# Optimization experiments

Hardware: AMD Instinct MI355X
Metric: run time of the kernel (lower is better)

Reference implementation:

```python
import jax, jax.numpy as jnp
import numpy as np

IN_DIM = 128
HID = 128
OUT = 128

def _linear(x, W, b):
    return x @ W + b

def setup_inputs() -> dict:
    key = jax.random.key(0)
    ks = jax.random.split(key, 16)
    B, N = 2, 512
    def w(k, fan_in, fan_out):
        lim = 1.0 / np.sqrt(fan_in)
        return jax.random.uniform(k, (fan_in, fan_out), jnp.float32, -lim, lim)
    def bvec(k, fan_in, fan_out):
        lim = 1.0 / np.sqrt(fan_in)
        return jax.random.uniform(k, (fan_out,), jnp.float32, -lim, lim)
    return {
        "features": jax.random.normal(ks[0], (B, N, IN_DIM), jnp.float32),
        "coords": jax.random.normal(ks[1], (B, N, 3), jnp.float32),
        "eW1": w(ks[2], 2 * IN_DIM + 1, HID), "eb1": bvec(ks[3], 2 * IN_DIM + 1, HID),
        "eW2": w(ks[4], HID, HID), "eb2": bvec(ks[5], HID, HID),
        "nW1": w(ks[6], IN_DIM + HID, HID), "nb1": bvec(ks[7], IN_DIM + HID, HID),
        "nW2": w(ks[8], HID, OUT), "nb2": bvec(ks[9], HID, OUT),
        "cW1": w(ks[10], HID, HID), "cb1": bvec(ks[11], HID, HID),
        "cW2": w(ks[12], HID, 1), "cb2": bvec(ks[13], HID, 1),
    }

def reference(features, coords, eW1, eb1, eW2, eb2, nW1, nb1, nW2, nb2, cW1, cb1, cW2, cb2):
    B, N, D = features.shape
    # pairwise coordinate differences and distances: (B, N, N, 3), (B, N, N, 1)
    coord_diff = coords[:, :, None, :] - coords[:, None, :, :]
    distances = jnp.sqrt(jnp.sum(coord_diff ** 2, axis=-1, keepdims=True) + 1e-8)
    # all-pairs edge features: (B, N, N, 2D+1)
    feat_i = jnp.broadcast_to(features[:, :, None, :], (B, N, N, D))
    feat_j = jnp.broadcast_to(features[:, None, :, :], (B, N, N, D))
    edge_features = jnp.concatenate([feat_i, feat_j, distances], axis=-1)
    edge_hidden = _linear(jax.nn.silu(_linear(edge_features, eW1, eb1)), eW2, eb2)
    # mean over neighbors j -> (B, N, HID)
    aggregated = jnp.mean(edge_hidden, axis=2)
    node_input = jnp.concatenate([features, aggregated], axis=-1)
    updated_features = _linear(jax.nn.silu(_linear(node_input, nW1, nb1)), nW2, nb2)
    # coordinate update
    coord_weights = _linear(jax.nn.silu(_linear(edge_hidden, cW1, cb1)), cW2, cb2)  # (B,N,N,1)
    updated_coords = coords + jnp.mean(coord_weights * coord_diff, axis=2)
    return (updated_features, updated_coords)
```

## Files before the change

kernel.cpp:

```cpp
#include <hip/hip_runtime.h>
#include <hip/hip_bf16.h>
#include <math.h>


typedef float f32x4 __attribute__((ext_vector_type(4)));
typedef short short8 __attribute__((ext_vector_type(8)));

#define MFMA16(a, b, c) __builtin_amdgcn_mfma_f32_16x16x32_bf16((a), (b), (c), 0, 0, 0)

__device__ __forceinline__ short f2bf(float x) {
    __hip_bfloat16 h = __float2bfloat16(x);
    union { __hip_bfloat16 h; short s; } v; v.h = h;
    return v.s;
}
__device__ __forceinline__ float bf2f(short s) {
    union { unsigned u; float f; } v; v.u = ((unsigned)(unsigned short)s) << 16;
    return v.f;
}
__device__ __forceinline__ float silu_f(float x) {
    return x * __builtin_amdgcn_rcpf(1.0f + __expf(-x));
}

__device__ __forceinline__ int swz(int row, int col) {
    int byte = (row << 8) | (col << 1);
    byte ^= (row & 7) << 4;
    return byte >> 1;
}

__global__ void egnn_prew(const float* __restrict__ feat, const float* __restrict__ eW1,
                          const float* __restrict__ eb1,
                          const float* __restrict__ eW2, const float* __restrict__ cW1,
                          const float* __restrict__ eb2, const float* __restrict__ cb1,
                          float* __restrict__ Abuf, float* __restrict__ Bbuf,
                          unsigned short* __restrict__ MbfT, float* __restrict__ bias2ws,
                          float* __restrict__ aggpart, float* __restrict__ coordpart,
                          int* __restrict__ done) {
    const int bid = blockIdx.x;
    const int t = threadIdx.x;
    if (bid < 1024) {
        __shared__ float f[128];
        if (t < 128) f[t] = feat[bid * 128 + t];
        __syncthreads();
        const int col  = t & 127;
        const int half = t >> 7;
        const float* W = eW1 + (size_t)half * 128 * 128 + col;
        float acc = half ? 0.f : eb1[col];
        #pragma unroll 8
        for (int k = 0; k < 128; ++k) acc += f[k] * W[(size_t)k * 128];
        if (half == 0) Abuf[bid * 128 + col] = acc;
        else           Bbuf[bid * 128 + col] = acc;
        if (t < 128) aggpart[(size_t)bid * 128 + t] = 0.f;
        if (t < 3)   coordpart[bid * 3 + t] = 0.f;
        if (t == 0)  done[bid] = 0;
    } else {
        const int idx = (bid - 1024) * 2 + (t >> 7);
        const int c = t & 127;
        if (idx < 128) {
            float acc = 0.f;
            #pragma unroll 8
            for (int h = 0; h < 128; ++h) acc += eW2[idx * 128 + h] * cW1[h * 128 + c];
            MbfT[c * 128 + idx] = (unsigned short)f2bf(acc);
        } else if (idx == 128) {
            float acc = cb1[c];
            #pragma unroll 8
            for (int h = 0; h < 128; ++h) acc += eb2[h] * cW1[h * 128 + c];
            bias2ws[c] = acc;
        }
    }
}

__global__ void __launch_bounds__(256, 2) egnn_main(
    const float* __restrict__ features, const float* __restrict__ coords,
    const float* __restrict__ eW1, const float* __restrict__ eW2,
    const float* __restrict__ eb2,
    const float* __restrict__ nW1, const float* __restrict__ nb1,
    const float* __restrict__ nW2, const float* __restrict__ nb2,
    const float* __restrict__ cW2, const float* __restrict__ cb2,
    const float* __restrict__ Abuf, const float* __restrict__ Bbuf,
    const unsigned short* __restrict__ MbfT, const float* __restrict__ bias2ws,
    float* __restrict__ aggpart, float* __restrict__ coordpart,
    int* __restrict__ done,
    float* __restrict__ out_feat, float* __restrict__ out_coord)
{
    constexpr int Nn = 512;
    __shared__ __align__(16) short se[64 * 128];
    __shared__ float aw[128], wd[128];
    __shared__ float cdp[2][3][64];
    __shared__ float warr[2][4][64];
    __shared__ float aggred[16][128];
    __shared__ float cred[4][3];
    __shared__ float ci3[3];
    __shared__ float pfi[128], paggh[128], phbuf[128], ppart[128], pcd[3];
    __shared__ int lastflag;

    const int tid  = threadIdx.x;
    const int lane = tid & 63;
    const int wave = tid >> 6;
    const int bid  = blockIdx.x;
    const int node = bid >> 1;
    const int half = bid & 1;
    const int b    = node >> 9;

    if (tid < 128) {
        aw[tid] = Abuf[node * 128 + tid];
        wd[tid] = eW1[256 * 128 + tid];
    }
    if (tid == 0) {
        ci3[0] = coords[node * 3 + 0];
        ci3[1] = coords[node * 3 + 1];
        ci3[2] = coords[node * 3 + 2];
    }

    const int cfrag = wave * 32 + (lane & 15);
    const int koff  = (lane >> 4) * 8;
    short8 wfM[2][4];
    #pragma unroll
    for (int n2 = 0; n2 < 2; ++n2)
        #pragma unroll
        for (int k = 0; k < 4; ++k)
            wfM[n2][k] = *(const short8*)&MbfT[(size_t)(cfrag + n2 * 16) * 128 + k * 32 + koff];
    __syncthreads();

    const float b2_0  = bias2ws[cfrag], b2_1 = bias2ws[cfrag + 16];
    const float cw2_0 = cW2[cfrag],     cw2_1 = cW2[cfrag + 16];
    const float cb2v  = cb2[0];
    const float cix = ci3[0], ciy = ci3[1], ciz = ci3[2];

    const int jr = tid >> 2, cb = (tid & 3) * 32;
    const int rg = tid >> 4, c8 = (tid & 15) * 8;

    float ap[8];
    #pragma unroll
    for (int q = 0; q < 8; ++q) ap[q] = 0.f;
    float cax = 0.f, cay = 0.f, caz = 0.f;

    for (int t = 0; t < 4; ++t) {
        const int par = t & 1;
        {
            const int j = half * 256 + t * 64 + jr;
            const float dx = cix - coords[(b * Nn + j) * 3 + 0];
            const float dy = ciy - coords[(b * Nn + j) * 3 + 1];
            const float dz = ciz - coords[(b * Nn + j) * 3 + 2];
            const float dj = sqrtf(dx * dx + dy * dy + dz * dz + 1e-8f);
            if ((tid & 3) == 0) {
                cdp[par][0][jr] = dx; cdp[par][1][jr] = dy; cdp[par][2][jr] = dz;
            }
            const float* Bj = Bbuf + (size_t)(b * Nn + j) * 128 + cb;
            #pragma unroll
            for (int cc = 0; cc < 32; cc += 8) {
                f32x4 x0 = *(const f32x4*)(Bj + cc);
                f32x4 x1 = *(const f32x4*)(Bj + cc + 4);
                short8 v;
                #pragma unroll
                for (int r = 0; r < 4; ++r) {
                    const int c = cb + cc + r;
                    v[r] = f2bf(silu_f(aw[c] + x0[r] + dj * wd[c]));
                }
                #pragma unroll
                for (int r = 0; r < 4; ++r) {
                    const int c = cb + cc + 4 + r;
                    v[4 + r] = f2bf(silu_f(aw[c] + x1[r] + dj * wd[c]));
                }
                *(short8*)&se[swz(jr, cb + cc)] = v;
            }
        }
        __syncthreads();

        f32x4 acc[4][2];
        #pragma unroll
        for (int m = 0; m < 4; ++m) {
            acc[m][0] = (f32x4){b2_0, b2_0, b2_0, b2_0};
            acc[m][1] = (f32x4){b2_1, b2_1, b2_1, b2_1};
        }
        #pragma unroll
        for (int m = 0; m < 4; ++m)
            #pragma unroll
            for (int k = 0; k < 4; ++k) {
                short8 a = *(const short8*)&se[swz(m * 16 + (lane & 15), k * 32 + koff)];
                acc[m][0] = MFMA16(a, wfM[0][k], acc[m][0]);
                acc[m][1] = MFMA16(a, wfM[1][k], acc[m][1]);
            }

        #pragma unroll
        for (int r = 0; r < 4; ++r) {
            short8 v = *(const short8*)&se[swz(rg * 4 + r, c8)];
            #pragma unroll
            for (int q = 0; q < 8; ++q) ap[q] += bf2f(v[q]);
        }

        #pragma unroll
        for (int m = 0; m < 4; ++m)
            #pragma unroll
            for (int reg = 0; reg < 4; ++reg) {
                float v = silu_f(acc[m][0][reg]) * cw2_0
                        + silu_f(acc[m][1][reg]) * cw2_1;
                v += __shfl_xor(v, 1); v += __shfl_xor(v, 2);
                v += __shfl_xor(v, 4); v += __shfl_xor(v, 8);
                if ((lane & 15) == 0)
                    warr[par][wave][m * 16 + (lane >> 4) * 4 + reg] = v;
            }
        __syncthreads();

        if (lane < 16) {
            const int row = wave * 16 + lane;
            const float w = warr[par][0][row] + warr[par][1][row]
                          + warr[par][2][row] + warr[par][3][row] + cb2v;
            cax += w * cdp[par][0][row];
            cay += w * cdp[par][1][row];
            caz += w * cdp[par][2][row];
        }
    }

    #pragma unroll
    for (int q = 0; q < 8; ++q) aggred[rg][c8 + q] = ap[q];
    {
        float sx = cax, sy = cay, sz = caz;
        sx += __shfl_xor(sx, 1); sy += __shfl_xor(sy, 1); sz += __shfl_xor(sz, 1);
        sx += __shfl_xor(sx, 2); sy += __shfl_xor(sy, 2); sz += __shfl_xor(sz, 2);
        sx += __shfl_xor(sx, 4); sy += __shfl_xor(sy, 4); sz += __shfl_xor(sz, 4);
        sx += __shfl_xor(sx, 8); sy += __shfl_xor(sy, 8); sz += __shfl_xor(sz, 8);
        if (lane == 0) { cred[wave][0] = sx; cred[wave][1] = sy; cred[wave][2] = sz; }
    }
    __syncthreads();
    if (tid < 128) {
        float s = 0.f;
        #pragma unroll
        for (int g = 0; g < 16; ++g) s += aggred[g][tid];
        atomicAdd(&aggpart[(size_t)node * 128 + tid], s);
    }
    if (tid < 3) {
        atomicAdd(&coordpart[node * 3 + tid],
                  cred[0][tid] + cred[1][tid] + cred[2][tid] + cred[3][tid]);
    }
    __syncthreads();
    if (tid == 0)
        lastflag = (atomicAdd(&done[node], 1) == 1) ? 1 : 0;
    __syncthreads();

    if (lastflag) {
        const int c = tid & 127, g = tid >> 7;
        if (tid < 128) {
            ppart[tid] = atomicAdd(&aggpart[(size_t)node * 128 + tid], 0.f);
            pfi[tid]   = features[node * 128 + tid];
        }
        if (tid < 3) pcd[tid] = atomicAdd(&coordpart[node * 3 + tid], 0.f);
        __syncthreads();
        if (tid < 3)
            out_coord[node * 3 + tid] = ci3[tid] + pcd[tid] * (1.f / 512.f);
        {
            float acc2 = 0.f;
            #pragma unroll 8
            for (int k = g * 64; k < g * 64 + 64; ++k) acc2 += ppart[k] * eW2[k * 128 + c];
            __syncthreads();
            if (g == 1) phbuf[c] = acc2;
            __syncthreads();
            if (g == 0) paggh[c] = (acc2 + phbuf[c]) * (1.f / 512.f) + eb2[c];
            __syncthreads();
        }
        {
            float acc2 = (g == 0) ? nb1[c] : 0.f;
            const float* src = (g == 0) ? pfi : paggh;
            const float* W = nW1 + (size_t)(g << 7) * 128 + c;
            #pragma unroll 8
            for (int k = 0; k < 128; ++k) acc2 += src[k] * W[(size_t)k * 128];
            if (g == 1) ppart[c] = acc2;
            __syncthreads();
            if (g == 0) phbuf[c] = silu_f(acc2 + ppart[c]);
            __syncthreads();
        }
        {
            float acc2 = (g == 0) ? nb2[c] : 0.f;
            #pragma unroll 8
            for (int k = g * 64; k < g * 64 + 64; ++k) acc2 += phbuf[k] * nW2[k * 128 + c];
            if (g == 1) ppart[c] = acc2;
            __syncthreads();
            if (g == 0) out_feat[node * 128 + c] = acc2 + ppart[c];
        }
    }
}

extern "C" void kernel_launch(void* const* d_in, const int* in_sizes, int n_in,
                              void* d_out, int out_size, void* d_ws, size_t ws_size,
                              hipStream_t stream)
{
    const float* features = (const float*)d_in[0];
    const float* coords   = (const float*)d_in[1];
    const float* eW1 = (const float*)d_in[2];
    const float* eb1 = (const float*)d_in[3];
    const float* eW2 = (const float*)d_in[4];
    const float* eb2 = (const float*)d_in[5];
    const float* nW1 = (const float*)d_in[6];
    const float* nb1 = (const float*)d_in[7];
    const float* nW2 = (const float*)d_in[8];
    const float* nb2 = (const float*)d_in[9];
    const float* cW1 = (const float*)d_in[10];
    const float* cb1 = (const float*)d_in[11];
    const float* cW2 = (const float*)d_in[12];
    const float* cb2 = (const float*)d_in[13];

    float* out = (float*)d_out;
    float* out_feat  = out;
    float* out_coord = out + 2 * 512 * 128;

    float* Abuf      = (float*)d_ws;
    float* Bbuf      = Abuf + 2 * 512 * 128;
    unsigned short* MbfT = (unsigned short*)(Bbuf + 2 * 512 * 128);
    float* bias2ws   = (float*)(MbfT + 128 * 128);
    float* aggpart   = bias2ws + 128;
    float* coordpart = aggpart + 1024 * 128;
    int*   done      = (int*)(coordpart + 1024 * 3);

    egnn_prew<<<1089, 256, 0, stream>>>(features, eW1, eb1, eW2, cW1, eb2, cb1,
                                        Abuf, Bbuf, MbfT, bias2ws,
                                        aggpart, coordpart, done);
    egnn_main<<<2048, 256, 0, stream>>>(features, coords, eW1, eW2, eb2,
                                        nW1, nb1, nW2, nb2, cW2, cb2,
                                        Abuf, Bbuf, MbfT, bias2ws,
                                        aggpart, coordpart, done,
                                        out_feat, out_coord);
}
```

Baseline: 191.3 us.

## Process each node in one 512-thread block instead of split halves with atomics

Main kernel now uses one 512-thread block per node, with eight waves covering 128 neighbor rows per tile, instead of two 256-thread blocks per node. The global atomic partial sums, done counters and last-block tail are removed, and the node MLP runs directly in every block using four thread groups. Shared memory is aliased to hold the larger tile. This drops the cross-block atomics and the zero-init work in the pre kernel, but halves the grid to 1024 blocks and raises per-block LDS use, which may lower occupancy.

```diff
diff --git a/kernel.cpp b/kernel.cpp
--- a/kernel.cpp
+++ b/kernel.cpp
@@ -32,9 +32,7 @@
                           const float* __restrict__ eW2, const float* __restrict__ cW1,
                           const float* __restrict__ eb2, const float* __restrict__ cb1,
                           float* __restrict__ Abuf, float* __restrict__ Bbuf,
-                          unsigned short* __restrict__ MbfT, float* __restrict__ bias2ws,
-                          float* __restrict__ aggpart, float* __restrict__ coordpart,
-                          int* __restrict__ done) {
+                          unsigned short* __restrict__ MbfT, float* __restrict__ bias2ws) {
     const int bid = blockIdx.x;
     const int t = threadIdx.x;
     if (bid < 1024) {
@@ -49,9 +47,6 @@
         for (int k = 0; k < 128; ++k) acc += f[k] * W[(size_t)k * 128];
         if (half == 0) Abuf[bid * 128 + col] = acc;
         else           Bbuf[bid * 128 + col] = acc;
-        if (t < 128) aggpart[(size_t)bid * 128 + t] = 0.f;
-        if (t < 3)   coordpart[bid * 3 + t] = 0.f;
-        if (t == 0)  done[bid] = 0;
     } else {
         const int idx = (bid - 1024) * 2 + (t >> 7);
         const int c = t & 127;
@@ -69,7 +64,7 @@
     }
 }
 
-__global__ void __launch_bounds__(256, 2) egnn_main(
+__global__ void __launch_bounds__(512) egnn_main(
     const float* __restrict__ features, const float* __restrict__ coords,
     const float* __restrict__ eW1, const float* __restrict__ eW2,
     const float* __restrict__ eb2,
@@ -78,27 +73,26 @@
     const float* __restrict__ cW2, const float* __restrict__ cb2,
     const float* __restrict__ Abuf, const float* __restrict__ Bbuf,
     const unsigned short* __restrict__ MbfT, const float* __restrict__ bias2ws,
-    float* __restrict__ aggpart, float* __restrict__ coordpart,
-    int* __restrict__ done,
     float* __restrict__ out_feat, float* __restrict__ out_coord)
 {
     constexpr int Nn = 512;
-    __shared__ __align__(16) short se[64 * 128];
+    __shared__ __align__(16) short se[128 * 128];
+    __shared__ __align__(16) float dynbuf[1792];
     __shared__ float aw[128], wd[128];
-    __shared__ float cdp[2][3][64];
-    __shared__ float warr[2][4][64];
-    __shared__ float aggred[16][128];
-    __shared__ float cred[4][3];
+    __shared__ float aggs[128], aggh[128], hbuf[128];
+    __shared__ float cred[8][3];
     __shared__ float ci3[3];
-    __shared__ float pfi[128], paggh[128], phbuf[128], ppart[128], pcd[3];
-    __shared__ int lastflag;
+
+    float (*cdp)[3][128]  = reinterpret_cast<float(*)[3][128]>(dynbuf);
+    float (*warr)[4][128] = reinterpret_cast<float(*)[4][128]>(dynbuf + 768);
+    float (*aggred)[128]  = reinterpret_cast<float(*)[128]>(se);
+    float (*part)[128]    = reinterpret_cast<float(*)[128]>(dynbuf);
+    float* pfi = dynbuf + 512;
 
     const int tid  = threadIdx.x;
     const int lane = tid & 63;
     const int wave = tid >> 6;
-    const int bid  = blockIdx.x;
-    const int node = bid >> 1;
-    const int half = bid & 1;
+    const int node = blockIdx.x;
     const int b    = node >> 9;
 
     if (tid < 128) {
@@ -111,8 +105,11 @@
         ci3[2] = coords[node * 3 + 2];
     }
 
-    const int cfrag = wave * 32 + (lane & 15);
+    const int r0 = (wave >> 2) * 64;
+    const int c0 = (wave & 3) * 32;
+    const int cfrag = c0 + (lane & 15);
     const int koff  = (lane >> 4) * 8;
+
     short8 wfM[2][4];
     #pragma unroll
     for (int n2 = 0; n2 < 2; ++n2)
@@ -137,7 +134,7 @@
     for (int t = 0; t < 4; ++t) {
         const int par = t & 1;
         {
-            const int j = half * 256 + t * 64 + jr;
+            const int j = t * 128 + jr;
             const float dx = cix - coords[(b * Nn + j) * 3 + 0];
             const float dy = ciy - coords[(b * Nn + j) * 3 + 1];
             const float dz = ciz - coords[(b * Nn + j) * 3 + 2];
@@ -176,7 +173,7 @@
         for (int m = 0; m < 4; ++m)
             #pragma unroll
             for (int k = 0; k < 4; ++k) {
-                short8 a = *(const short8*)&se[swz(m * 16 + (lane & 15), k * 32 + koff)];
+                short8 a = *(const short8*)&se[swz(r0 + m * 16 + (lane & 15), k * 32 + koff)];
                 acc[m][0] = MFMA16(a, wfM[0][k], acc[m][0]);
                 acc[m][1] = MFMA16(a, wfM[1][k], acc[m][1]);
             }
@@ -197,7 +194,7 @@
                 v += __shfl_xor(v, 1); v += __shfl_xor(v, 2);
                 v += __shfl_xor(v, 4); v += __shfl_xor(v, 8);
                 if ((lane & 15) == 0)
-                    warr[par][wave][m * 16 + (lane >> 4) * 4 + reg] = v;
+                    warr[par][wave & 3][r0 + m * 16 + (lane >> 4) * 4 + reg] = v;
             }
         __syncthreads();
 
@@ -222,60 +219,54 @@
         if (lane == 0) { cred[wave][0] = sx; cred[wave][1] = sy; cred[wave][2] = sz; }
     }
     __syncthreads();
+
+    const int c = tid & 127, g = tid >> 7;
     if (tid < 128) {
         float s = 0.f;
         #pragma unroll
-        for (int g = 0; g < 16; ++g) s += aggred[g][tid];
-        atomicAdd(&aggpart[(size_t)node * 128 + tid], s);
+        for (int gg = 0; gg < 32; ++gg) s += aggred[gg][tid];
+        aggs[tid] = s;
+        pfi[tid]  = features[node * 128 + tid];
     }
     if (tid < 3) {
-        atomicAdd(&coordpart[node * 3 + tid],
-                  cred[0][tid] + cred[1][tid] + cred[2][tid] + cred[3][tid]);
+        float s = 0.f;
+        #pragma unroll
+        for (int w = 0; w < 8; ++w) s += cred[w][tid];
+        out_coord[node * 3 + tid] = ci3[tid] + s * (1.f / 512.f);
     }
     __syncthreads();
-    if (tid == 0)
-        lastflag = (atomicAdd(&done[node], 1) == 1) ? 1 : 0;
-    __syncthreads();
-
-    if (lastflag) {
-        const int c = tid & 127, g = tid >> 7;
-        if (tid < 128) {
-            ppart[tid] = atomicAdd(&aggpart[(size_t)node * 128 + tid], 0.f);
-            pfi[tid]   = features[node * 128 + tid];
-        }
-        if (tid < 3) pcd[tid] = atomicAdd(&coordpart[node * 3 + tid], 0.f);
-        __syncthreads();
-        if (tid < 3)
-            out_coord[node * 3 + tid] = ci3[tid] + pcd[tid] * (1.f / 512.f);
-        {
-            float acc2 = 0.f;
+
+    {
+        float a2 = 0.f;
+        #pragma unroll 8
+        for (int k = g * 32; k < g * 32 + 32; ++k) a2 += aggs[k] * eW2[k * 128 + c];
+        if (g) part[g][c] = a2;
+        __syncthreads();
+        if (!g) aggh[c] = (a2 + part[1][c] + part[2][c] + part[3][c]) * (1.f / 512.f) + eb2[c];
+        __syncthreads();
+    }
+    {
+        float a2 = (g == 0) ? nb1[c] : 0.f;
+        if (g < 2) {
             #pragma unroll 8
-            for (int k = g * 64; k < g * 64 + 64; ++k) acc2 += ppart[k] * eW2[k * 128 + c];
-            __syncthreads();
-            if (g == 1) phbuf[c] = acc2;
-            __syncthreads();
-            if (g == 0) paggh[c] = (acc2 + phbuf[c]) * (1.f / 512.f) + eb2[c];
-            __syncthreads();
-        }
-        {
-            float acc2 = (g == 0) ? nb1[c] : 0.f;
-            const float* src = (g == 0) ? pfi : paggh;
-            const float* W = nW1 + (size_t)(g << 7) * 128 + c;
+            for (int k = g * 64; k < g * 64 + 64; ++k) a2 += pfi[k] * nW1[k * 128 + c];
+        } else {
             #pragma unroll 8
-            for (int k = 0; k < 128; ++k) acc2 += src[k] * W[(size_t)k * 128];
-            if (g == 1) ppart[c] = acc2;
-            __syncthreads();
-            if (g == 0) phbuf[c] = silu_f(acc2 + ppart[c]);
-            __syncthreads();
-        }
-        {
-            float acc2 = (g == 0) ? nb2[c] : 0.f;
-            #pragma unroll 8
-            for (int k = g * 64; k < g * 64 + 64; ++k) acc2 += phbuf[k] * nW2[k * 128 + c];
-            if (g == 1) ppart[c] = acc2;
-            __syncthreads();
-            if (g == 0) out_feat[node * 128 + c] = acc2 + ppart[c];
-        }
+            for (int k = (g - 2) * 64; k < (g - 2) * 64 + 64; ++k)
+                a2 += aggh[k] * nW1[(128 + k) * 128 + c];
+        }
+        if (g) part[g][c] = a2;
+        __syncthreads();
+        if (!g) hbuf[c] = silu_f(a2 + part[1][c] + part[2][c] + part[3][c]);
+        __syncthreads();
+    }
+    {
+        float a2 = (g == 0) ? nb2[c] : 0.f;
+        #pragma unroll 8
+        for (int k = g * 32; k < g * 32 + 32; ++k) a2 += hbuf[k] * nW2[k * 128 + c];
+        if (g) part[g][c] = a2;
+        __syncthreads();
+        if (!g) out_feat[node * 128 + c] = a2 + part[1][c] + part[2][c] + part[3][c];
     }
 }
 
@@ -306,16 +297,11 @@
     float* Bbuf      = Abuf + 2 * 512 * 128;
     unsigned short* MbfT = (unsigned short*)(Bbuf + 2 * 512 * 128);
     float* bias2ws   = (float*)(MbfT + 128 * 128);
-    float* aggpart   = bias2ws + 128;
-    float* coordpart = aggpart + 1024 * 128;
-    int*   done      = (int*)(coordpart + 1024 * 3);
 
     egnn_prew<<<1089, 256, 0, stream>>>(features, eW1, eb1, eW2, cW1, eb2, cb1,
-                                        Abuf, Bbuf, MbfT, bias2ws,
-                                        aggpart, coordpart, done);
-    egnn_main<<<2048, 256, 0, stream>>>(features, coords, eW1, eW2, eb2,
+                                        Abuf, Bbuf, MbfT, bias2ws);
+    egnn_main<<<1024, 512, 0, stream>>>(features, coords, eW1, eW2, eb2,
                                         nW1, nb1, nW2, nb2, cW2, cb2,
                                         Abuf, Bbuf, MbfT, bias2ws,
-                                        aggpart, coordpart, done,
                                         out_feat, out_coord);
 }
```

After: 214.2 us. 1.12x slower.
